# Performance work log

Measured on AMD Instinct MI355X. Metric: run time of the kernel, lower is better.

## Reference

```python
import jax, jax.numpy as jnp
import numpy as np

BN_EPS = 1e-5


def setup_inputs() -> dict:
    key = jax.random.key(0)
    k_x, k_A, k_W, k_b = jax.random.split(key, 4)
    N, C_in, T, V = 32, 64, 300, 25
    P, C_out = 3, 128
    x = jax.random.normal(k_x, (N, C_in, T, V), dtype=jnp.float32)
    # adjacency partitions: nonnegative, row-normalized-ish (rand in [0,1))
    A = jax.random.uniform(k_A, (P, V, V), dtype=jnp.float32)
    # kaiming fan_in init for 1x1 conv weights: std = sqrt(2/fan_in)
    W = jax.random.normal(k_W, (P, C_out, C_in), dtype=jnp.float32) * np.sqrt(2.0 / C_in)
    b = jax.random.normal(k_b, (P, C_out), dtype=jnp.float32) * 0.01
    gamma = jnp.ones((C_out,), dtype=jnp.float32)
    beta = jnp.zeros((C_out,), dtype=jnp.float32)
    return {"x": x, "A": A, "W": W, "b": b, "gamma": gamma, "beta": beta}


def reference(x, A, W, b, gamma, beta):
    # x: (N, C, T, V); A: (P, V, V); W: (P, C_out, C_in); b: (P, C_out)
    # Per partition p: aggregate over graph (x @ A_p), then 1x1 conv, then sum over p.
    # Fused: y[n,o,t,v] = sum_p sum_c W[p,o,c] * (sum_w x[n,c,t,w] * A[p,w,v]) + sum_p b[p,o]
    xa = jnp.einsum('nctw,pwv->pnctv', x, A)            # (P, N, C_in, T, V)
    y = jnp.einsum('pnctv,poc->notv', xa, W)            # (N, C_out, T, V)
    y = y + jnp.sum(b, axis=0)[None, :, None, None]
    # BatchNorm2d, training-mode forward: stats over (N, T, V), biased variance
    mean = jnp.mean(y, axis=(0, 2, 3), keepdims=True)
    var = jnp.mean(jnp.square(y - mean), axis=(0, 2, 3), keepdims=True)
    y = (y - mean) * jax.lax.rsqrt(var + BN_EPS)
    y = y * gamma[None, :, None, None] + beta[None, :, None, None]
    return jax.nn.relu(y)
```

## Files before the change

### kernel.cpp

```cpp
#include <hip/hip_runtime.h>
#include <hip/hip_bf16.h>

#define NN 32
#define CIN 64
#define TTOT 300
#define VV 25
#define PP 3
#define COUT 128
#define TTILE 5
#define NTILES 60
#define CNT 240000.0f

#define XSTR 40
#define ZSTR 72
#define NCOLP 160

#define WS_STATS 0
#define WS_SCALE 256
#define WS_SHIFT 384
#define WS_BSUM  512
#define WS_W2    640

typedef float f32x4 __attribute__((ext_vector_type(4)));
typedef short s16x8 __attribute__((ext_vector_type(8)));

__device__ __forceinline__ short f2bf(float f) {
    unsigned u = __float_as_uint(f);
    u += 0x7fff + ((u >> 16) & 1);
    return (short)(u >> 16);
}

__global__ __launch_bounds__(256) void prep_kernel(const float* __restrict__ W,
                                                   const float* __restrict__ b,
                                                   float* __restrict__ ws) {
    int tid = blockIdx.x * blockDim.x + threadIdx.x;
    if (tid < 256) ws[WS_STATS + tid] = 0.0f;
    if (tid >= 256 && tid < 384) {
        int o = tid - 256;
        ws[WS_BSUM + o] = b[o] + b[COUT + o] + b[2 * COUT + o];
    }
    if (tid < COUT * 192) {
        int o = tid / 192, k = tid % 192;
        int p = k / 64, c = k % 64;
        ((short*)(ws + WS_W2))[tid] = f2bf(W[(p * COUT + o) * CIN + c]);
    }
}

__global__ __launch_bounds__(512, 4) void sgcn_main(const float* __restrict__ x,
                                                    const float* __restrict__ A,
                                                    float* __restrict__ y,
                                                    float* ws) {
    __shared__ __align__(16) short Xs[TTILE * 64 * XSTR];
    __shared__ __align__(16) short Ats[PP * 32 * XSTR];
    __shared__ __align__(16) short Z2s[NCOLP * ZSTR];
    __shared__ float sstat[256];

    const int tid  = threadIdx.x;
    const int lane = tid & 63;
    const int wave = tid >> 6;
    const int n  = blockIdx.x / NTILES;
    const int t0 = (blockIdx.x % NTILES) * TTILE;
    const int lg = lane >> 4;
    const int li = lane & 15;

    {
        int* az = (int*)Ats;
        #pragma unroll
        for (int i = 0; i < 4; ++i) {
            int idx = tid + i * 512;
            if (idx < PP * 32 * XSTR / 2) az[idx] = 0;
        }
        if (tid < 256) sstat[tid] = 0.0f;
    }
    __syncthreads();

    if (tid < 320) {
        int c = tid / 5, t = tid % 5;
        const float* xp = x + ((size_t)(n * CIN + c) * TTOT + (t0 + t)) * VV;
        short* dst = &Xs[(t * 64 + c) * XSTR];
        #pragma unroll
        for (int g = 0; g < 5; ++g) {
            s16x8 v;
            #pragma unroll
            for (int e = 0; e < 8; ++e) {
                int w = g * 8 + e;
                v[e] = (w < VV) ? f2bf(xp[w]) : (short)0;
            }
            *(s16x8*)(dst + g * 8) = v;
        }
    }
    for (int i = tid; i < PP * VV * VV; i += 512) {
        int v = i % VV, w = (i / VV) % VV, p = i / (VV * VV);
        Ats[(p * 32 + v) * XSTR + w] = f2bf(A[i]);
    }
    __syncthreads();

    const int ow = wave >> 1;
    const int cw = wave & 1;
    const int o0 = ow * 32;
    const short* w2 = (const short*)(ws + WS_W2);

    f32x4 acc[2][5];
    #pragma unroll
    for (int mf = 0; mf < 2; ++mf)
        #pragma unroll
        for (int cf = 0; cf < 5; ++cf)
            acc[mf][cf] = (f32x4){0.f, 0.f, 0.f, 0.f};

    for (int p = 0; p < PP; ++p) {
        s16x8 wf[2][2];
        #pragma unroll
        for (int mf = 0; mf < 2; ++mf)
            #pragma unroll
            for (int ks = 0; ks < 2; ++ks)
                wf[mf][ks] = *(const s16x8*)(w2 + (o0 + mf * 16 + li) * 192
                                                + p * 64 + ks * 32 + lg * 8);

        #pragma unroll
        for (int q = 0; q < 5; ++q) {
            int f = wave * 5 + q;
            int t = f >> 3, rem = f & 7;
            int vf = rem >> 2, cfr = rem & 3;
            s16x8 af = *(const s16x8*)(&Ats[(p * 32 + vf * 16 + li) * XSTR + lg * 8]);
            s16x8 bf = *(const s16x8*)(&Xs[(t * 64 + cfr * 16 + li) * XSTR + lg * 8]);
            f32x4 z = (f32x4){0.f, 0.f, 0.f, 0.f};
            f32x4 d = __builtin_amdgcn_mfma_f32_16x16x32_bf16(af, bf, z, 0, 0, 0);
            int brow = t * 32 + vf * 16 + lg * 4;
            int ccol = cfr * 16 + li;
            #pragma unroll
            for (int r = 0; r < 4; ++r)
                Z2s[(brow + r) * ZSTR + ccol] = f2bf(d[r]);
        }
        __syncthreads();

        #pragma unroll
        for (int cf = 0; cf < 5; ++cf) {
            int col0 = cw * 80 + cf * 16;
            #pragma unroll
            for (int ks = 0; ks < 2; ++ks) {
                s16x8 zf = *(const s16x8*)(&Z2s[(col0 + li) * ZSTR + ks * 32 + lg * 8]);
                #pragma unroll
                for (int mf = 0; mf < 2; ++mf)
                    acc[mf][cf] = __builtin_amdgcn_mfma_f32_16x16x32_bf16(
                        wf[mf][ks], zf, acc[mf][cf], 0, 0, 0);
            }
        }
        __syncthreads();
    }

    const float* bsum = ws + WS_BSUM;
    #pragma unroll
    for (int mf = 0; mf < 2; ++mf) {
        #pragma unroll
        for (int r = 0; r < 4; ++r) {
            int o = o0 + mf * 16 + lg * 4 + r;
            float bo = bsum[o];
            float s = 0.f, sq = 0.f;
            #pragma unroll
            for (int cf = 0; cf < 5; ++cf) {
                int colp = cw * 80 + cf * 16 + li;
                int t = colp >> 5, v = colp & 31;
                float val = acc[mf][cf][r] + bo;
                if (v < VV) {
                    y[((size_t)(n * COUT + o) * TTOT + (t0 + t)) * VV + v] = val;
                    s += val; sq += val * val;
                }
            }
            #pragma unroll
            for (int m = 1; m < 16; m <<= 1) {
                s  += __shfl_xor(s, m, 64);
                sq += __shfl_xor(sq, m, 64);
            }
            if (li == 0) {
                atomicAdd(&sstat[o], s);
                atomicAdd(&sstat[128 + o], sq);
            }
        }
    }
    __syncthreads();
    if (tid < 256) atomicAdd(&ws[WS_STATS + tid], sstat[tid]);
}

__global__ void finalize_kernel(const float* __restrict__ gamma,
                                const float* __restrict__ beta,
                                float* ws) {
    int o = threadIdx.x;
    float mean = ws[WS_STATS + o] * (1.0f / CNT);
    float ex2  = ws[WS_STATS + 128 + o] * (1.0f / CNT);
    float var  = ex2 - mean * mean;
    float rstd = rsqrtf(var + 1e-5f);
    float sc = gamma[o] * rstd;
    ws[WS_SCALE + o] = sc;
    ws[WS_SHIFT + o] = beta[o] - mean * sc;
}

__global__ __launch_bounds__(256) void norm_relu_kernel(float* __restrict__ y,
                                                        const float* __restrict__ ws) {
    const int total8 = (NN * COUT * TTOT * VV) / 8;
    const float* scale = ws + WS_SCALE;
    const float* shift = ws + WS_SHIFT;
    for (int i = blockIdx.x * blockDim.x + threadIdx.x; i < total8;
         i += gridDim.x * blockDim.x) {
        size_t base = (size_t)i * 8;
        int row0 = (int)(base / 7500);
        int row1 = (int)((base + 7) / 7500);
        int o0 = row0 & 127, o1 = row1 & 127;
        float s0 = scale[o0], h0 = shift[o0];
        float s1 = scale[o1], h1 = shift[o1];
        size_t bnd = (size_t)(row0 + 1) * 7500;
        float4 a = *(const float4*)(y + base);
        float4 b = *(const float4*)(y + base + 4);
        float vals[8] = {a.x, a.y, a.z, a.w, b.x, b.y, b.z, b.w};
        #pragma unroll
        for (int e = 0; e < 8; ++e) {
            bool first = (base + (size_t)e) < bnd;
            float s = first ? s0 : s1;
            float h = first ? h0 : h1;
            vals[e] = fmaxf(vals[e] * s + h, 0.0f);
        }
        a = make_float4(vals[0], vals[1], vals[2], vals[3]);
        b = make_float4(vals[4], vals[5], vals[6], vals[7]);
        *(float4*)(y + base) = a;
        *(float4*)(y + base + 4) = b;
    }
}

extern "C" void kernel_launch(void* const* d_in, const int* in_sizes, int n_in,
                              void* d_out, int out_size, void* d_ws, size_t ws_size,
                              hipStream_t stream) {
    const float* x     = (const float*)d_in[0];
    const float* A     = (const float*)d_in[1];
    const float* W     = (const float*)d_in[2];
    const float* b     = (const float*)d_in[3];
    const float* gamma = (const float*)d_in[4];
    const float* beta  = (const float*)d_in[5];
    float* y  = (float*)d_out;
    float* ws = (float*)d_ws;

    prep_kernel<<<96, 256, 0, stream>>>(W, b, ws);
    sgcn_main<<<NN * NTILES, 512, 0, stream>>>(x, A, y, ws);
    finalize_kernel<<<1, 128, 0, stream>>>(gamma, beta, ws);
    norm_relu_kernel<<<2048, 256, 0, stream>>>(y, ws);
}
```

Measured before the change: 137.4 us.

## Pack Z columns densely to cut second-GEMM work and coalesce x loads

Stores the intermediate Z tile with (t,v) columns packed densely as t*25+v instead of padding each t to 32. The 125 valid columns then fit in 128, so each wave computes 4 column fragments instead of 5 and skips the padding MFMAs. The x tile load is rewritten so consecutive threads read consecutive elements, which coalesces global reads. The occupancy hint rises to 6 blocks per SM, and the padding rows of Z are zeroed once. Output stores now need a division by 25 per column, and the higher occupancy target may constrain registers.

```diff
diff --git a/kernel.cpp b/kernel.cpp
--- a/kernel.cpp
+++ b/kernel.cpp
@@ -13,7 +13,7 @@
 
 #define XSTR 40
 #define ZSTR 72
-#define NCOLP 160
+#define ZROWS 128
 
 #define WS_STATS 0
 #define WS_SCALE 256
@@ -46,15 +46,14 @@
     }
 }
 
-__global__ __launch_bounds__(512, 4) void sgcn_main(const float* __restrict__ x,
+__global__ __launch_bounds__(512, 6) void sgcn_main(const float* __restrict__ x,
                                                     const float* __restrict__ A,
                                                     float* __restrict__ y,
                                                     float* ws) {
     __shared__ __align__(16) short Xs[TTILE * 64 * XSTR];
     __shared__ __align__(16) short Ats[PP * 32 * XSTR];
-    __shared__ __align__(16) short Z2s[NCOLP * ZSTR];
+    __shared__ __align__(16) short Z2s[ZROWS * ZSTR];
     __shared__ float sstat[256];
-
     const int tid  = threadIdx.x;
     const int lane = tid & 63;
     const int wave = tid >> 6;
@@ -70,28 +69,26 @@
             int idx = tid + i * 512;
             if (idx < PP * 32 * XSTR / 2) az[idx] = 0;
         }
+        if (tid < 108) ((int*)(Z2s + 125 * ZSTR))[tid] = 0;
         if (tid < 256) sstat[tid] = 0.0f;
     }
     __syncthreads();
 
-    if (tid < 320) {
-        int c = tid / 5, t = tid % 5;
-        const float* xp = x + ((size_t)(n * CIN + c) * TTOT + (t0 + t)) * VV;
-        short* dst = &Xs[(t * 64 + c) * XSTR];
-        #pragma unroll
-        for (int g = 0; g < 5; ++g) {
-            s16x8 v;
-            #pragma unroll
-            for (int e = 0; e < 8; ++e) {
-                int w = g * 8 + e;
-                v[e] = (w < VV) ? f2bf(xp[w]) : (short)0;
-            }
-            *(s16x8*)(dst + g * 8) = v;
-        }
-    }
-    for (int i = tid; i < PP * VV * VV; i += 512) {
-        int v = i % VV, w = (i / VV) % VV, p = i / (VV * VV);
-        Ats[(p * 32 + v) * XSTR + w] = f2bf(A[i]);
+    {
+        const float* xb = x + (size_t)n * (CIN * TTOT * VV) + (size_t)t0 * VV;
+        #pragma unroll
+        for (int it = 0; it < 20; ++it) {
+            int i = tid + it * 512;
+            int c = i / 160;
+            int r2 = i - c * 160;
+            int t = r2 >> 5, w = r2 & 31;
+            float val = (w < VV) ? xb[c * (TTOT * VV) + t * VV + w] : 0.0f;
+            Xs[(t * 64 + c) * XSTR + w] = f2bf(val);
+        }
+        for (int i = tid; i < PP * VV * VV; i += 512) {
+            int v = i % VV, w = (i / VV) % VV, p = i / (VV * VV);
+            Ats[(p * 32 + v) * XSTR + w] = f2bf(A[i]);
+        }
     }
     __syncthreads();
 
@@ -100,11 +97,11 @@
     const int o0 = ow * 32;
     const short* w2 = (const short*)(ws + WS_W2);
 
-    f32x4 acc[2][5];
+    f32x4 acc[2][4];
     #pragma unroll
     for (int mf = 0; mf < 2; ++mf)
         #pragma unroll
-        for (int cf = 0; cf < 5; ++cf)
+        for (int cf = 0; cf < 4; ++cf)
             acc[mf][cf] = (f32x4){0.f, 0.f, 0.f, 0.f};
 
     for (int p = 0; p < PP; ++p) {
@@ -125,17 +122,19 @@
             s16x8 bf = *(const s16x8*)(&Xs[(t * 64 + cfr * 16 + li) * XSTR + lg * 8]);
             f32x4 z = (f32x4){0.f, 0.f, 0.f, 0.f};
             f32x4 d = __builtin_amdgcn_mfma_f32_16x16x32_bf16(af, bf, z, 0, 0, 0);
-            int brow = t * 32 + vf * 16 + lg * 4;
+            int m0 = vf * 16 + lg * 4;
             int ccol = cfr * 16 + li;
             #pragma unroll
-            for (int r = 0; r < 4; ++r)
-                Z2s[(brow + r) * ZSTR + ccol] = f2bf(d[r]);
+            for (int r = 0; r < 4; ++r) {
+                int m = m0 + r;
+                if (m < VV) Z2s[(t * VV + m) * ZSTR + ccol] = f2bf(d[r]);
+            }
         }
         __syncthreads();
 
         #pragma unroll
-        for (int cf = 0; cf < 5; ++cf) {
-            int col0 = cw * 80 + cf * 16;
+        for (int cf = 0; cf < 4; ++cf) {
+            int col0 = cw * 64 + cf * 16;
             #pragma unroll
             for (int ks = 0; ks < 2; ++ks) {
                 s16x8 zf = *(const s16x8*)(&Z2s[(col0 + li) * ZSTR + ks * 32 + lg * 8]);
@@ -157,11 +156,12 @@
             float bo = bsum[o];
             float s = 0.f, sq = 0.f;
             #pragma unroll
-            for (int cf = 0; cf < 5; ++cf) {
-                int colp = cw * 80 + cf * 16 + li;
-                int t = colp >> 5, v = colp & 31;
+            for (int cf = 0; cf < 4; ++cf) {
+                int col = cw * 64 + cf * 16 + li;
                 float val = acc[mf][cf][r] + bo;
-                if (v < VV) {
+                if (col < TTILE * VV) {
+                    int t = col / VV;
+                    int v = col - t * VV;
                     y[((size_t)(n * COUT + o) * TTOT + (t0 + t)) * VV + v] = val;
                     s += val; sq += val * val;
                 }
```

After: 181.3 us. 32.0% more time.
